# Kernel tuning notes

Measured on AMD Instinct MI355X. Metric: run time of the kernel, lower is better.

Reference implementation:

```python
import jax, jax.numpy as jnp
import numpy as np

T = 4096      # tokens (batch*seq)
D = 1024      # hidden_size
F = 4096      # intermediate_size
E = 8         # num_local_experts


def setup_inputs() -> dict:
    key = jax.random.key(0)
    ks = jax.random.split(key, 6)
    scale_in = 1.0 / np.sqrt(D)
    scale_f = 1.0 / np.sqrt(F)
    return {
        "x": jax.random.normal(ks[0], (T, D), jnp.float32),
        "gate_w": jax.random.normal(ks[1], (E, D), jnp.float32) * scale_in,
        "gate_b": jnp.zeros((E,), jnp.float32),
        "w1": jax.random.normal(ks[2], (E, F, D), jnp.float32) * scale_in,
        "w3": jax.random.normal(ks[3], (E, F, D), jnp.float32) * scale_in,
        "w2": jax.random.normal(ks[4], (E, D, F), jnp.float32) * scale_f,
        "top_k": 2,
    }


def reference(x, gate_w, gate_b, w1, w3, w2, top_k):
    # --- routing: gate linear -> softmax -> top-k, renormalized ---
    logits = x @ gate_w.T + gate_b                     # [T, E]
    probs = jax.nn.softmax(logits, axis=-1)            # [T, E]
    topk_p, topk_i = jax.lax.top_k(probs, top_k)       # [T, k]
    topk_p = topk_p / jnp.sum(topk_p, axis=-1, keepdims=True)
    # dense combine weights [T, E]: zeros except selected experts
    cw = jnp.zeros((x.shape[0], gate_w.shape[0]), x.dtype)
    cw = cw.at[jnp.arange(x.shape[0])[:, None], topk_i].set(topk_p)
    # --- experts: SwiGLU FFN, computed densely per expert, masked combine ---
    h1 = jnp.einsum('td,efd->etf', x, w1)              # [E, T, F]
    h3 = jnp.einsum('td,efd->etf', x, w3)              # [E, T, F]
    act = jax.nn.silu(h1) * h3                         # [E, T, F]
    expert_out = jnp.einsum('etf,edf->etd', act, w2)   # [E, T, D]
    out = jnp.einsum('etd,te->td', expert_out, cw)     # [T, D]
    return out
```

## Files before the change

### kernel.cpp

```cpp
#include <hip/hip_runtime.h>
#include <hip/hip_bf16.h>

#define T_TOK 4096
#define DIM   1024
#define FDIM  4096
#define NEXP  8
#define BM    128
#define BN    64
#define BK    32
#define LDP   40

typedef __attribute__((ext_vector_type(8))) short bf16x8_t;
typedef __attribute__((ext_vector_type(4))) float f32x4_t;

__device__ __forceinline__ unsigned short f2bf(float f) {
    union { __hip_bfloat16 h; unsigned short u; } c;
    c.h = __float2bfloat16(f);
    return c.u;
}
__device__ __forceinline__ ushort4 cvt8(const float4& a, const float4& b) {
    ushort4 q;
    q.x = f2bf(a.x); q.y = f2bf(a.y); q.z = f2bf(a.z); q.w = f2bf(a.w);
    (void)b; return q;
}

__global__ __launch_bounds__(256) void gate_kernel(
    const float* __restrict__ x, const float* __restrict__ gw,
    const float* __restrict__ gb, int* __restrict__ cnt,
    int* __restrict__ toklist, float* __restrict__ wlist)
{
    const int lane = threadIdx.x & 63;
    const int wv   = threadIdx.x >> 6;
    const int t    = blockIdx.x * 4 + wv;
    const float* xr = x + (size_t)t * DIM;

    float4 xv[4];
#pragma unroll
    for (int c = 0; c < 4; ++c)
        xv[c] = *reinterpret_cast<const float4*>(xr + c * 256 + lane * 4);

    float logit[NEXP];
#pragma unroll
    for (int e = 0; e < NEXP; ++e) {
        const float* gr = gw + e * DIM;
        float s = 0.f;
#pragma unroll
        for (int c = 0; c < 4; ++c) {
            float4 g = *reinterpret_cast<const float4*>(gr + c * 256 + lane * 4);
            s += xv[c].x * g.x + xv[c].y * g.y + xv[c].z * g.z + xv[c].w * g.w;
        }
#pragma unroll
        for (int o = 32; o > 0; o >>= 1) s += __shfl_xor(s, o, 64);
        logit[e] = s + gb[e];
    }

    if (lane == 0) {
        int i1 = 0;
#pragma unroll
        for (int e = 1; e < NEXP; ++e) if (logit[e] > logit[i1]) i1 = e;
        int i2 = (i1 == 0) ? 1 : 0;
#pragma unroll
        for (int e = 0; e < NEXP; ++e)
            if (e != i1 && e != i2 && logit[e] > logit[i2]) i2 = e;
        float eb = expf(logit[i2] - logit[i1]);
        float wA = 1.f / (1.f + eb);
        float wB = eb / (1.f + eb);
        int p = atomicAdd(&cnt[i1], 1);
        toklist[i1 * T_TOK + p] = t; wlist[i1 * T_TOK + p] = wA;
        p = atomicAdd(&cnt[i2], 1);
        toklist[i2 * T_TOK + p] = t; wlist[i2 * T_TOK + p] = wB;
    }
}

__global__ void offsets_kernel(const int* __restrict__ cnt, int* __restrict__ offs)
{
    if (threadIdx.x == 0) {
        int o = 0;
#pragma unroll
        for (int e = 0; e < NEXP; ++e) {
            offs[e] = o;
            o += ((cnt[e] + BM - 1) / BM) * BM;
        }
    }
}

__global__ __launch_bounds__(256) void gather_kernel(
    const float* __restrict__ x, const int* __restrict__ cnt,
    const int* __restrict__ offs, const int* __restrict__ toklist,
    unsigned short* __restrict__ Xp)
{
    const int b = blockIdx.x;
    const int e = b >> 12;
    const int i = b & 4095;
    const int c  = cnt[e];
    const int ca = ((c + BM - 1) >> 7) << 7;
    if (i >= ca) return;
    unsigned short* dst = Xp + (size_t)(offs[e] + i) * DIM;
    const int t4 = threadIdx.x * 4;
    ushort4 o;
    if (i < c) {
        const float* src = x + (size_t)toklist[e * T_TOK + i] * DIM;
        float4 v = *reinterpret_cast<const float4*>(src + t4);
        o.x = f2bf(v.x); o.y = f2bf(v.y); o.z = f2bf(v.z); o.w = f2bf(v.w);
    } else {
        o.x = 0; o.y = 0; o.z = 0; o.w = 0;
    }
    *reinterpret_cast<ushort4*>(dst + t4) = o;
}

__global__ __launch_bounds__(256, 3) void stageA_kernel(
    const unsigned short* __restrict__ Xp, const float* __restrict__ w1,
    const float* __restrict__ w3, const int* __restrict__ cnt,
    const int* __restrict__ offs, unsigned short* __restrict__ act)
{
    const int e  = blockIdx.z;
    const int c  = cnt[e];
    const int mt = blockIdx.y;
    if (mt * BM >= c) return;
    const int nt = blockIdx.x;
    const size_t slot0 = (size_t)offs[e] + (size_t)mt * BM;
    const int n0 = nt * BN;

    __shared__ __align__(16) unsigned short As[BM * LDP];
    __shared__ __align__(16) unsigned short B1s[BN * LDP];
    __shared__ __align__(16) unsigned short B3s[BN * LDP];

    const int tid  = threadIdx.x;
    const int lane = tid & 63;
    const int wv   = tid >> 6;
    const int wm   = (wv & 1) * 64;
    const int wn   = (wv >> 1) * 32;
    const int quad = lane >> 4;
    const int r    = lane & 15;

    const int arow = tid >> 1;
    const int acol = (tid & 1) * 16;
    const unsigned short* Ag = Xp + (slot0 + arow) * DIM + acol;
    unsigned short* Asw = As + arow * LDP + acol;
    const int brow = tid >> 2;
    const int bcol = (tid & 3) * 8;
    const float* B1g = w1 + ((size_t)e * FDIM + n0 + brow) * DIM + bcol;
    const float* B3g = w3 + ((size_t)e * FDIM + n0 + brow) * DIM + bcol;
    unsigned short* B1w = B1s + brow * LDP + bcol;
    unsigned short* B3w = B3s + brow * LDP + bcol;

    f32x4_t acc1[4][2];
    f32x4_t acc3[4][2];
#pragma unroll
    for (int i = 0; i < 4; ++i)
#pragma unroll
        for (int j = 0; j < 2; ++j) {
            acc1[i][j] = (f32x4_t){0.f, 0.f, 0.f, 0.f};
            acc3[i][j] = (f32x4_t){0.f, 0.f, 0.f, 0.f};
        }

    uint4  a0 = *reinterpret_cast<const uint4*>(Ag);
    uint4  a1 = *reinterpret_cast<const uint4*>(Ag + 8);
    float4 p10 = *reinterpret_cast<const float4*>(B1g);
    float4 p11 = *reinterpret_cast<const float4*>(B1g + 4);
    float4 p30 = *reinterpret_cast<const float4*>(B3g);
    float4 p31 = *reinterpret_cast<const float4*>(B3g + 4);

    for (int k0 = 0; k0 < DIM; k0 += BK) {
        *reinterpret_cast<uint4*>(Asw)     = a0;
        *reinterpret_cast<uint4*>(Asw + 8) = a1;
        ushort4 q;
        q.x = f2bf(p10.x); q.y = f2bf(p10.y); q.z = f2bf(p10.z); q.w = f2bf(p10.w);
        *reinterpret_cast<ushort4*>(B1w)     = q;
        q.x = f2bf(p11.x); q.y = f2bf(p11.y); q.z = f2bf(p11.z); q.w = f2bf(p11.w);
        *reinterpret_cast<ushort4*>(B1w + 4) = q;
        q.x = f2bf(p30.x); q.y = f2bf(p30.y); q.z = f2bf(p30.z); q.w = f2bf(p30.w);
        *reinterpret_cast<ushort4*>(B3w)     = q;
        q.x = f2bf(p31.x); q.y = f2bf(p31.y); q.z = f2bf(p31.z); q.w = f2bf(p31.w);
        *reinterpret_cast<ushort4*>(B3w + 4) = q;
        __syncthreads();

        if (k0 + BK < DIM) {
            a0  = *reinterpret_cast<const uint4*>(Ag + k0 + BK);
            a1  = *reinterpret_cast<const uint4*>(Ag + k0 + BK + 8);
            p10 = *reinterpret_cast<const float4*>(B1g + k0 + BK);
            p11 = *reinterpret_cast<const float4*>(B1g + k0 + BK + 4);
            p30 = *reinterpret_cast<const float4*>(B3g + k0 + BK);
            p31 = *reinterpret_cast<const float4*>(B3g + k0 + BK + 4);
        }

        bf16x8_t af[4];
#pragma unroll
        for (int i = 0; i < 4; ++i)
            af[i] = *reinterpret_cast<const bf16x8_t*>(As + (wm + i * 16 + r) * LDP + quad * 8);
#pragma unroll
        for (int j = 0; j < 2; ++j) {
            bf16x8_t b1 = *reinterpret_cast<const bf16x8_t*>(B1s + (wn + j * 16 + r) * LDP + quad * 8);
            bf16x8_t b3 = *reinterpret_cast<const bf16x8_t*>(B3s + (wn + j * 16 + r) * LDP + quad * 8);
#pragma unroll
            for (int i = 0; i < 4; ++i) {
                acc1[i][j] = __builtin_amdgcn_mfma_f32_16x16x32_bf16(af[i], b1, acc1[i][j], 0, 0, 0);
                acc3[i][j] = __builtin_amdgcn_mfma_f32_16x16x32_bf16(af[i], b3, acc3[i][j], 0, 0, 0);
            }
        }
        __syncthreads();
    }

    unsigned short* abase = act + slot0 * FDIM + n0;
#pragma unroll
    for (int i = 0; i < 4; ++i)
#pragma unroll
        for (int j = 0; j < 2; ++j)
#pragma unroll
            for (int rr = 0; rr < 4; ++rr) {
                int m = wm + i * 16 + quad * 4 + rr;
                int n = wn + j * 16 + r;
                float h1 = acc1[i][j][rr];
                float h3 = acc3[i][j][rr];
                float sw = h1 / (1.f + __expf(-h1)) * h3;
                abase[(size_t)m * FDIM + n] = f2bf(sw);
            }
}

__global__ __launch_bounds__(256, 4) void stageB_kernel(
    const unsigned short* __restrict__ act, const float* __restrict__ w2,
    const int* __restrict__ cnt, const int* __restrict__ offs,
    const int* __restrict__ toklist, const float* __restrict__ wlist,
    float* __restrict__ out)
{
    const int e  = blockIdx.z;
    const int c  = cnt[e];
    const int mt = blockIdx.y;
    if (mt * BM >= c) return;
    const int nt = blockIdx.x;
    const size_t slot0 = (size_t)offs[e] + (size_t)mt * BM;
    const int n0 = nt * BN;

    __shared__ __align__(16) unsigned short As[BM * LDP];
    __shared__ __align__(16) unsigned short Bs[BN * LDP];

    const int tid  = threadIdx.x;
    const int lane = tid & 63;
    const int wv   = tid >> 6;
    const int wm   = (wv & 1) * 64;
    const int wn   = (wv >> 1) * 32;
    const int quad = lane >> 4;
    const int r    = lane & 15;

    const int arow = tid >> 1;
    const int acol = (tid & 1) * 16;
    const unsigned short* Ag = act + (slot0 + arow) * FDIM + acol;
    unsigned short* Asw = As + arow * LDP + acol;
    const int brow = tid >> 2;
    const int bcol = (tid & 3) * 8;
    const float* Bg = w2 + ((size_t)e * DIM + n0 + brow) * FDIM + bcol;
    unsigned short* Bw = Bs + brow * LDP + bcol;

    f32x4_t acc[4][2];
#pragma unroll
    for (int i = 0; i < 4; ++i)
#pragma unroll
        for (int j = 0; j < 2; ++j) acc[i][j] = (f32x4_t){0.f, 0.f, 0.f, 0.f};

    uint4  a0 = *reinterpret_cast<const uint4*>(Ag);
    uint4  a1 = *reinterpret_cast<const uint4*>(Ag + 8);
    float4 p0 = *reinterpret_cast<const float4*>(Bg);
    float4 p1 = *reinterpret_cast<const float4*>(Bg + 4);

    for (int k0 = 0; k0 < FDIM; k0 += BK) {
        *reinterpret_cast<uint4*>(Asw)     = a0;
        *reinterpret_cast<uint4*>(Asw + 8) = a1;
        ushort4 q;
        q.x = f2bf(p0.x); q.y = f2bf(p0.y); q.z = f2bf(p0.z); q.w = f2bf(p0.w);
        *reinterpret_cast<ushort4*>(Bw)     = q;
        q.x = f2bf(p1.x); q.y = f2bf(p1.y); q.z = f2bf(p1.z); q.w = f2bf(p1.w);
        *reinterpret_cast<ushort4*>(Bw + 4) = q;
        __syncthreads();

        if (k0 + BK < FDIM) {
            a0 = *reinterpret_cast<const uint4*>(Ag + k0 + BK);
            a1 = *reinterpret_cast<const uint4*>(Ag + k0 + BK + 8);
            p0 = *reinterpret_cast<const float4*>(Bg + k0 + BK);
            p1 = *reinterpret_cast<const float4*>(Bg + k0 + BK + 4);
        }

        bf16x8_t af[4];
#pragma unroll
        for (int i = 0; i < 4; ++i)
            af[i] = *reinterpret_cast<const bf16x8_t*>(As + (wm + i * 16 + r) * LDP + quad * 8);
#pragma unroll
        for (int j = 0; j < 2; ++j) {
            bf16x8_t bf = *reinterpret_cast<const bf16x8_t*>(Bs + (wn + j * 16 + r) * LDP + quad * 8);
#pragma unroll
            for (int i = 0; i < 4; ++i)
                acc[i][j] = __builtin_amdgcn_mfma_f32_16x16x32_bf16(af[i], bf, acc[i][j], 0, 0, 0);
        }
        __syncthreads();
    }

    const int row0 = mt * BM;
#pragma unroll
    for (int i = 0; i < 4; ++i)
#pragma unroll
        for (int rr = 0; rr < 4; ++rr) {
            int m = wm + i * 16 + quad * 4 + rr;
            int row = row0 + m;
            if (row < c) {
                int tok  = toklist[e * T_TOK + row];
                float wt = wlist[e * T_TOK + row];
                float* orow = out + (size_t)tok * DIM + n0;
#pragma unroll
                for (int j = 0; j < 2; ++j) {
                    int n = wn + j * 16 + r;
                    atomicAdd(&orow[n], wt * acc[i][j][rr]);
                }
            }
        }
}

extern "C" void kernel_launch(void* const* d_in, const int* in_sizes, int n_in,
                              void* d_out, int out_size, void* d_ws, size_t ws_size,
                              hipStream_t stream)
{
    (void)in_sizes; (void)n_in; (void)out_size; (void)ws_size;
    const float* x  = (const float*)d_in[0];
    const float* gw = (const float*)d_in[1];
    const float* gb = (const float*)d_in[2];
    const float* w1 = (const float*)d_in[3];
    const float* w3 = (const float*)d_in[4];
    const float* w2 = (const float*)d_in[5];
    float* out = (float*)d_out;

    char* ws = (char*)d_ws;
    unsigned short* Xp  = (unsigned short*)ws;
    unsigned short* act = (unsigned short*)(ws + 18874368);
    int*   cnt     = (int*)(ws + 18874368 + 75497472);
    int*   offs    = cnt + 64;
    int*   toklist = cnt + 128;
    float* wlist   = (float*)(cnt + 128 + NEXP * T_TOK);

    hipMemsetAsync(cnt, 0, 64, stream);
    hipMemsetAsync(out, 0, (size_t)T_TOK * DIM * sizeof(float), stream);

    gate_kernel<<<T_TOK / 4, 256, 0, stream>>>(x, gw, gb, cnt, toklist, wlist);
    offsets_kernel<<<1, 64, 0, stream>>>(cnt, offs);
    gather_kernel<<<NEXP * T_TOK, 256, 0, stream>>>(x, cnt, offs, toklist, Xp);
    stageA_kernel<<<dim3(FDIM / BN, T_TOK / BM, NEXP), 256, 0, stream>>>(Xp, w1, w3, cnt, offs, act);
    stageB_kernel<<<dim3(DIM / BN, T_TOK / BM, NEXP), 256, 0, stream>>>(act, w2, cnt, offs, toklist, wlist, out);
}
```

Baseline: 880.0 us.

## Double-buffer LDS with direct global-to-LDS loads; widen and split-K stage B

Both expert GEMM stages now use double-buffered shared memory. Activation tiles go straight from global memory into LDS via global_load_lds, and the bf16-converted weight tiles are written into the next buffer after the MFMAs, so one barrier per K step replaces two. Stage B widens its N tile to 128, splits K in two across the grid, and relies on the existing atomic accumulation to combine the halves. The cost is the unpadded LDS layout, which may cause bank conflicts, more atomics into the output, and more register pressure in stage B.

New measurement: 917.2 us. +4.2%, slower.

```diff
diff --git a/kernel.cpp b/kernel.cpp
--- a/kernel.cpp
+++ b/kernel.cpp
@@ -6,22 +6,27 @@
 #define FDIM  4096
 #define NEXP  8
 #define BM    128
-#define BN    64
 #define BK    32
-#define LDP   40
+#define BN_A  64
+#define BN_B  128
 
 typedef __attribute__((ext_vector_type(8))) short bf16x8_t;
 typedef __attribute__((ext_vector_type(4))) float f32x4_t;
+
+#define GLD16(gp, lp) __builtin_amdgcn_global_load_lds( \
+    (const __attribute__((address_space(1))) unsigned int*)(gp), \
+    (__attribute__((address_space(3))) unsigned int*)(lp), 16, 0, 0)
 
 __device__ __forceinline__ unsigned short f2bf(float f) {
     union { __hip_bfloat16 h; unsigned short u; } c;
     c.h = __float2bfloat16(f);
     return c.u;
 }
-__device__ __forceinline__ ushort4 cvt8(const float4& a, const float4& b) {
-    ushort4 q;
-    q.x = f2bf(a.x); q.y = f2bf(a.y); q.z = f2bf(a.z); q.w = f2bf(a.w);
-    (void)b; return q;
+__device__ __forceinline__ uint4 pack8(const float4& a, const float4& b) {
+    union { unsigned short s[8]; uint4 v; } u;
+    u.s[0] = f2bf(a.x); u.s[1] = f2bf(a.y); u.s[2] = f2bf(a.z); u.s[3] = f2bf(a.w);
+    u.s[4] = f2bf(b.x); u.s[5] = f2bf(b.y); u.s[6] = f2bf(b.z); u.s[7] = f2bf(b.w);
+    return u.v;
 }
 
 __global__ __launch_bounds__(256) void gate_kernel(
@@ -119,11 +124,11 @@
     if (mt * BM >= c) return;
     const int nt = blockIdx.x;
     const size_t slot0 = (size_t)offs[e] + (size_t)mt * BM;
-    const int n0 = nt * BN;
-
-    __shared__ __align__(16) unsigned short As[BM * LDP];
-    __shared__ __align__(16) unsigned short B1s[BN * LDP];
-    __shared__ __align__(16) unsigned short B3s[BN * LDP];
+    const int n0 = nt * BN_A;
+
+    __shared__ __align__(16) unsigned short As[2][BM * BK];
+    __shared__ __align__(16) unsigned short B1s[2][BN_A * BK];
+    __shared__ __align__(16) unsigned short B3s[2][BN_A * BK];
 
     const int tid  = threadIdx.x;
     const int lane = tid & 63;
@@ -133,16 +138,16 @@
     const int quad = lane >> 4;
     const int r    = lane & 15;
 
-    const int arow = tid >> 1;
-    const int acol = (tid & 1) * 16;
-    const unsigned short* Ag = Xp + (slot0 + arow) * DIM + acol;
-    unsigned short* Asw = As + arow * LDP + acol;
+    const int aRow = wv * 32 + (lane >> 2);
+    const unsigned short* Adma = Xp + (slot0 + aRow) * DIM + (lane & 3) * 8;
+    const int aLds0 = (wv * 32) * BK;
+    const int aLds1 = (wv * 32 + 16) * BK;
+
     const int brow = tid >> 2;
     const int bcol = (tid & 3) * 8;
     const float* B1g = w1 + ((size_t)e * FDIM + n0 + brow) * DIM + bcol;
     const float* B3g = w3 + ((size_t)e * FDIM + n0 + brow) * DIM + bcol;
-    unsigned short* B1w = B1s + brow * LDP + bcol;
-    unsigned short* B3w = B3s + brow * LDP + bcol;
+    const int bofs = brow * BK + bcol;
 
     f32x4_t acc1[4][2];
     f32x4_t acc3[4][2];
@@ -154,30 +159,23 @@
             acc3[i][j] = (f32x4_t){0.f, 0.f, 0.f, 0.f};
         }
 
-    uint4  a0 = *reinterpret_cast<const uint4*>(Ag);
-    uint4  a1 = *reinterpret_cast<const uint4*>(Ag + 8);
+    GLD16(Adma,            &As[0][aLds0]);
+    GLD16(Adma + 16 * DIM, &As[0][aLds1]);
     float4 p10 = *reinterpret_cast<const float4*>(B1g);
     float4 p11 = *reinterpret_cast<const float4*>(B1g + 4);
     float4 p30 = *reinterpret_cast<const float4*>(B3g);
     float4 p31 = *reinterpret_cast<const float4*>(B3g + 4);
-
-    for (int k0 = 0; k0 < DIM; k0 += BK) {
-        *reinterpret_cast<uint4*>(Asw)     = a0;
-        *reinterpret_cast<uint4*>(Asw + 8) = a1;
-        ushort4 q;
-        q.x = f2bf(p10.x); q.y = f2bf(p10.y); q.z = f2bf(p10.z); q.w = f2bf(p10.w);
-        *reinterpret_cast<ushort4*>(B1w)     = q;
-        q.x = f2bf(p11.x); q.y = f2bf(p11.y); q.z = f2bf(p11.z); q.w = f2bf(p11.w);
-        *reinterpret_cast<ushort4*>(B1w + 4) = q;
-        q.x = f2bf(p30.x); q.y = f2bf(p30.y); q.z = f2bf(p30.z); q.w = f2bf(p30.w);
-        *reinterpret_cast<ushort4*>(B3w)     = q;
-        q.x = f2bf(p31.x); q.y = f2bf(p31.y); q.z = f2bf(p31.z); q.w = f2bf(p31.w);
-        *reinterpret_cast<ushort4*>(B3w + 4) = q;
-        __syncthreads();
-
-        if (k0 + BK < DIM) {
-            a0  = *reinterpret_cast<const uint4*>(Ag + k0 + BK);
-            a1  = *reinterpret_cast<const uint4*>(Ag + k0 + BK + 8);
+    *reinterpret_cast<uint4*>(&B1s[0][bofs]) = pack8(p10, p11);
+    *reinterpret_cast<uint4*>(&B3s[0][bofs]) = pack8(p30, p31);
+    __syncthreads();
+
+    int kk = 0;
+    for (int k0 = 0; k0 < DIM; k0 += BK, kk ^= 1) {
+        const int nxt = kk ^ 1;
+        const bool more = (k0 + BK) < DIM;
+        if (more) {
+            GLD16(Adma + (k0 + BK),            &As[nxt][aLds0]);
+            GLD16(Adma + (k0 + BK) + 16 * DIM, &As[nxt][aLds1]);
             p10 = *reinterpret_cast<const float4*>(B1g + k0 + BK);
             p11 = *reinterpret_cast<const float4*>(B1g + k0 + BK + 4);
             p30 = *reinterpret_cast<const float4*>(B3g + k0 + BK);
@@ -187,16 +185,21 @@
         bf16x8_t af[4];
 #pragma unroll
         for (int i = 0; i < 4; ++i)
-            af[i] = *reinterpret_cast<const bf16x8_t*>(As + (wm + i * 16 + r) * LDP + quad * 8);
+            af[i] = *reinterpret_cast<const bf16x8_t*>(&As[kk][(wm + i * 16 + r) * BK + quad * 8]);
 #pragma unroll
         for (int j = 0; j < 2; ++j) {
-            bf16x8_t b1 = *reinterpret_cast<const bf16x8_t*>(B1s + (wn + j * 16 + r) * LDP + quad * 8);
-            bf16x8_t b3 = *reinterpret_cast<const bf16x8_t*>(B3s + (wn + j * 16 + r) * LDP + quad * 8);
+            bf16x8_t b1 = *reinterpret_cast<const bf16x8_t*>(&B1s[kk][(wn + j * 16 + r) * BK + quad * 8]);
+            bf16x8_t b3 = *reinterpret_cast<const bf16x8_t*>(&B3s[kk][(wn + j * 16 + r) * BK + quad * 8]);
 #pragma unroll
             for (int i = 0; i < 4; ++i) {
                 acc1[i][j] = __builtin_amdgcn_mfma_f32_16x16x32_bf16(af[i], b1, acc1[i][j], 0, 0, 0);
                 acc3[i][j] = __builtin_amdgcn_mfma_f32_16x16x32_bf16(af[i], b3, acc3[i][j], 0, 0, 0);
             }
+        }
+
+        if (more) {
+            *reinterpret_cast<uint4*>(&B1s[nxt][bofs]) = pack8(p10, p11);
+            *reinterpret_cast<uint4*>(&B3s[nxt][bofs]) = pack8(p30, p31);
         }
         __syncthreads();
     }
@@ -217,78 +220,89 @@
             }
 }
 
-__global__ __launch_bounds__(256, 4) void stageB_kernel(
+__global__ __launch_bounds__(256, 3) void stageB_kernel(
     const unsigned short* __restrict__ act, const float* __restrict__ w2,
     const int* __restrict__ cnt, const int* __restrict__ offs,
     const int* __restrict__ toklist, const float* __restrict__ wlist,
     float* __restrict__ out)
 {
-    const int e  = blockIdx.z;
+    const int e  = blockIdx.z & 7;
+    const int ks = blockIdx.z >> 3;
     const int c  = cnt[e];
     const int mt = blockIdx.y;
     if (mt * BM >= c) return;
     const int nt = blockIdx.x;
     const size_t slot0 = (size_t)offs[e] + (size_t)mt * BM;
-    const int n0 = nt * BN;
-
-    __shared__ __align__(16) unsigned short As[BM * LDP];
-    __shared__ __align__(16) unsigned short Bs[BN * LDP];
+    const int n0 = nt * BN_B;
+    const int kbase = ks * (FDIM / 2);
+    const int kend  = kbase + FDIM / 2;
+
+    __shared__ __align__(16) unsigned short As[2][BM * BK];
+    __shared__ __align__(16) unsigned short Bs[2][BN_B * BK];
 
     const int tid  = threadIdx.x;
     const int lane = tid & 63;
     const int wv   = tid >> 6;
     const int wm   = (wv & 1) * 64;
-    const int wn   = (wv >> 1) * 32;
+    const int wn   = (wv >> 1) * 64;
     const int quad = lane >> 4;
     const int r    = lane & 15;
 
-    const int arow = tid >> 1;
-    const int acol = (tid & 1) * 16;
-    const unsigned short* Ag = act + (slot0 + arow) * FDIM + acol;
-    unsigned short* Asw = As + arow * LDP + acol;
-    const int brow = tid >> 2;
-    const int bcol = (tid & 3) * 8;
-    const float* Bg = w2 + ((size_t)e * DIM + n0 + brow) * FDIM + bcol;
-    unsigned short* Bw = Bs + brow * LDP + bcol;
-
-    f32x4_t acc[4][2];
+    const int aRow = wv * 32 + (lane >> 2);
+    const unsigned short* Adma = act + (slot0 + aRow) * FDIM + kbase + (lane & 3) * 8;
+    const int aLds0 = (wv * 32) * BK;
+    const int aLds1 = (wv * 32 + 16) * BK;
+
+    const int brow = tid >> 1;
+    const int bcol = (tid & 1) * 16;
+    const float* Bg = w2 + ((size_t)e * DIM + n0 + brow) * FDIM + kbase + bcol;
+    const int bofs = brow * BK + bcol;
+
+    f32x4_t acc[4][4];
 #pragma unroll
     for (int i = 0; i < 4; ++i)
 #pragma unroll
-        for (int j = 0; j < 2; ++j) acc[i][j] = (f32x4_t){0.f, 0.f, 0.f, 0.f};
-
-    uint4  a0 = *reinterpret_cast<const uint4*>(Ag);
-    uint4  a1 = *reinterpret_cast<const uint4*>(Ag + 8);
+        for (int j = 0; j < 4; ++j) acc[i][j] = (f32x4_t){0.f, 0.f, 0.f, 0.f};
+
+    GLD16(Adma,            &As[0][aLds0]);
+    GLD16(Adma + 16 * FDIM, &As[0][aLds1]);
     float4 p0 = *reinterpret_cast<const float4*>(Bg);
     float4 p1 = *reinterpret_cast<const float4*>(Bg + 4);
-
-    for (int k0 = 0; k0 < FDIM; k0 += BK) {
-        *reinterpret_cast<uint4*>(Asw)     = a0;
-        *reinterpret_cast<uint4*>(Asw + 8) = a1;
-        ushort4 q;
-        q.x = f2bf(p0.x); q.y = f2bf(p0.y); q.z = f2bf(p0.z); q.w = f2bf(p0.w);
-        *reinterpret_cast<ushort4*>(Bw)     = q;
-        q.x = f2bf(p1.x); q.y = f2bf(p1.y); q.z = f2bf(p1.z); q.w = f2bf(p1.w);
-        *reinterpret_cast<ushort4*>(Bw + 4) = q;
-        __syncthreads();
-
-        if (k0 + BK < FDIM) {
-            a0 = *reinterpret_cast<const uint4*>(Ag + k0 + BK);
-            a1 = *reinterpret_cast<const uint4*>(Ag + k0 + BK + 8);
-            p0 = *reinterpret_cast<const float4*>(Bg + k0 + BK);
-            p1 = *reinterpret_cast<const float4*>(Bg + k0 + BK + 4);
+    float4 p2 = *reinterpret_cast<const float4*>(Bg + 8);
+    float4 p3 = *reinterpret_cast<const float4*>(Bg + 12);
+    *reinterpret_cast<uint4*>(&Bs[0][bofs])     = pack8(p0, p1);
+    *reinterpret_cast<uint4*>(&Bs[0][bofs + 8]) = pack8(p2, p3);
+    __syncthreads();
+
+    int kk = 0;
+    for (int k0 = kbase; k0 < kend; k0 += BK, kk ^= 1) {
+        const int nxt = kk ^ 1;
+        const int kd = k0 - kbase;
+        const bool more = (k0 + BK) < kend;
+        if (more) {
+            GLD16(Adma + kd + BK,             &As[nxt][aLds0]);
+            GLD16(Adma + kd + BK + 16 * FDIM, &As[nxt][aLds1]);
+            p0 = *reinterpret_cast<const float4*>(Bg + kd + BK);
+            p1 = *reinterpret_cast<const float4*>(Bg + kd + BK + 4);
+            p2 = *reinterpret_cast<const float4*>(Bg + kd + BK + 8);
+            p3 = *reinterpret_cast<const float4*>(Bg + kd + BK + 12);
         }
 
         bf16x8_t af[4];
 #pragma unroll
         for (int i = 0; i < 4; ++i)
-            af[i] = *reinterpret_cast<const bf16x8_t*>(As + (wm + i * 16 + r) * LDP + quad * 8);
-#pragma unroll
-        for (int j = 0; j < 2; ++j) {
-            bf16x8_t bf = *reinterpret_cast<const bf16x8_t*>(Bs + (wn + j * 16 + r) * LDP + quad * 8);
+            af[i] = *reinterpret_cast<const bf16x8_t*>(&As[kk][(wm + i * 16 + r) * BK + quad * 8]);
+#pragma unroll
+        for (int j = 0; j < 4; ++j) {
+            bf16x8_t bf = *reinterpret_cast<const bf16x8_t*>(&Bs[kk][(wn + j * 16 + r) * BK + quad * 8]);
 #pragma unroll
             for (int i = 0; i < 4; ++i)
                 acc[i][j] = __builtin_amdgcn_mfma_f32_16x16x32_bf16(af[i], bf, acc[i][j], 0, 0, 0);
+        }
+
+        if (more) {
+            *reinterpret_cast<uint4*>(&Bs[nxt][bofs])     = pack8(p0, p1);
+            *reinterpret_cast<uint4*>(&Bs[nxt][bofs + 8]) = pack8(p2, p3);
         }
         __syncthreads();
     }
@@ -305,7 +319,7 @@
                 float wt = wlist[e * T_TOK + row];
                 float* orow = out + (size_t)tok * DIM + n0;
 #pragma unroll
-                for (int j = 0; j < 2; ++j) {
+                for (int j = 0; j < 4; ++j) {
                     int n = wn + j * 16 + r;
                     atomicAdd(&orow[n], wt * acc[i][j][rr]);
                 }
@@ -340,6 +354,6 @@
     gate_kernel<<<T_TOK / 4, 256, 0, stream>>>(x, gw, gb, cnt, toklist, wlist);
     offsets_kernel<<<1, 64, 0, stream>>>(cnt, offs);
     gather_kernel<<<NEXP * T_TOK, 256, 0, stream>>>(x, cnt, offs, toklist, Xp);
-    stageA_kernel<<<dim3(FDIM / BN, T_TOK / BM, NEXP), 256, 0, stream>>>(Xp, w1, w3, cnt, offs, act);
-    stageB_kernel<<<dim3(DIM / BN, T_TOK / BM, NEXP), 256, 0, stream>>>(act, w2, cnt, offs, toklist, wlist, out);
-}
+    stageA_kernel<<<dim3(FDIM / BN_A, T_TOK / BM, NEXP), 256, 0, stream>>>(Xp, w1, w3, cnt, offs, act);
+    stageB_kernel<<<dim3(DIM / BN_B, T_TOK / BM, NEXP * 2), 256, 0, stream>>>(act, w2, cnt, offs, toklist, wlist, out);
+}
```
